# Optimization experiments

Measured on AMD Instinct MI355X. Metric: run time of the kernel, lower is better.

## Reference

```python
import jax, jax.numpy as jnp
import numpy as np

UNITS = 1024
IN_DIM = 1024
B, T = 32, 2048


def setup_inputs() -> dict:
    key = jax.random.key(0)
    k1, k2, k3 = jax.random.split(key, 3)
    # glorot-uniform style scaling for weights
    lim_k = float(np.sqrt(6.0 / (IN_DIM + UNITS)))
    lim_r = float(np.sqrt(6.0 / (UNITS + UNITS)))
    x = jax.random.normal(k1, (B, T, IN_DIM), dtype=jnp.float32)
    kernel = jax.random.uniform(k2, (IN_DIM, UNITS), minval=-lim_k, maxval=lim_k, dtype=jnp.float32)
    recurrent_kernel = jax.random.uniform(k3, (UNITS, UNITS), minval=-lim_r, maxval=lim_r, dtype=jnp.float32)
    h0 = jnp.zeros((B, UNITS), dtype=jnp.float32)
    return {"x": x, "h0": h0, "kernel": kernel, "recurrent_kernel": recurrent_kernel}


def reference(x, h0, kernel, recurrent_kernel):
    # MinimalRNNCell: h_t = x_t @ W_in + h_{t-1} @ W_rec (purely linear, no activation)
    # Hoist the input projection out of the scan: one big GEMM over [B*T, IN_DIM].
    xin = jnp.einsum('btd,du->btu', x, kernel)  # [B, T, U]

    def step(h, xt):
        h_new = xt + h @ recurrent_kernel
        return h_new, None

    # scan over time axis; Keras RNN default returns the last output [B, U]
    h_last, _ = jax.lax.scan(step, h0, jnp.swapaxes(xin, 0, 1))
    return h_last
```

## Files before the change

### kernel.cpp

```cpp
#include <hip/hip_runtime.h>
#include <cstddef>
#include <cstdint>


namespace {

constexpr int BATCH = 32;
constexpr int T = 2048;
constexpr int U = 1024;
constexpr int LJ = 8;
constexpr int CJ = T / LJ;
constexpr int MJ = CJ * BATCH;

typedef _Float16 f16;
typedef _Float16 f16x4 __attribute__((ext_vector_type(4)));
typedef _Float16 f16x8 __attribute__((ext_vector_type(8)));
typedef float f32x4 __attribute__((ext_vector_type(4)));

__device__ inline void gload16(const void* g, void* l) {
    __builtin_amdgcn_global_load_lds(
        (const __attribute__((address_space(1))) unsigned int*)g,
        (__attribute__((address_space(3))) unsigned int*)l, 16, 0, 0);
}

__global__ __launch_bounds__(256)
void split_x(const float* __restrict__ x, f16* __restrict__ xh, long n4)
{
    long i = (long)blockIdx.x * 256 + threadIdx.x;
    const long stride = (long)gridDim.x * 256;
    for (; i < n4; i += stride) {
        const float4 v = *(const float4*)(x + i * 4);
        f16x4 h;
        h.x = (f16)v.x; h.y = (f16)v.y; h.z = (f16)v.z; h.w = (f16)v.w;
        *(f16x4*)(xh + i * 4) = h;
    }
}

__global__ __launch_bounds__(256)
void prep(const float* __restrict__ R, const float* __restrict__ W,
          const float* __restrict__ h0,
          f16* __restrict__ TTRh, f16* __restrict__ TTRl,
          f16* __restrict__ Rrh, f16* __restrict__ Rrl,
          f16* __restrict__ GhT, f16* __restrict__ GlT,
          f16* __restrict__ Wrh, f16* __restrict__ Wrl,
          f16* __restrict__ h0rh, f16* __restrict__ h0rl)
{
    const int z = blockIdx.z;
    const float* S = z ? W : R;
    f16* Dh = z ? GhT : TTRh;
    f16* Dl = z ? GlT : TTRl;
    const long dstride = z ? 8192 : 1024;
    const long doff = z ? 7168 : 0;
    f16* Rh_ = z ? Wrh : Rrh;
    f16* Rl_ = z ? Wrl : Rrl;

    __shared__ float tile[32][33];
    const int t = threadIdx.x;
    const int k0 = blockIdx.x * 32;
    const int n0 = blockIdx.y * 32;
    {
        const int r = t >> 3, c4 = (t & 7) << 2;
        const float4 v = *(const float4*)(S + (size_t)(k0 + r) * U + n0 + c4);
        tile[r][c4 + 0] = v.x; tile[r][c4 + 1] = v.y;
        tile[r][c4 + 2] = v.z; tile[r][c4 + 3] = v.w;
        f16x4 h, lo;
        h.x = (f16)v.x; lo.x = (f16)((v.x - (float)h.x) * 2048.0f);
        h.y = (f16)v.y; lo.y = (f16)((v.y - (float)h.y) * 2048.0f);
        h.z = (f16)v.z; lo.z = (f16)((v.z - (float)h.z) * 2048.0f);
        h.w = (f16)v.w; lo.w = (f16)((v.w - (float)h.w) * 2048.0f);
        const size_t ro = (size_t)(k0 + r) * U + n0 + c4;
        *(f16x4*)(Rh_ + ro) = h;
        *(f16x4*)(Rl_ + ro) = lo;
    }
    __syncthreads();
    {
        const int c = t >> 3, r4 = (t & 7) << 2;
        float v0 = tile[r4 + 0][c], v1 = tile[r4 + 1][c],
              v2 = tile[r4 + 2][c], v3 = tile[r4 + 3][c];
        f16x4 h, lo;
        h.x = (f16)v0; lo.x = (f16)((v0 - (float)h.x) * 2048.0f);
        h.y = (f16)v1; lo.y = (f16)((v1 - (float)h.y) * 2048.0f);
        h.z = (f16)v2; lo.z = (f16)((v2 - (float)h.z) * 2048.0f);
        h.w = (f16)v3; lo.w = (f16)((v3 - (float)h.w) * 2048.0f);
        const size_t o = (size_t)(n0 + c) * dstride + doff + k0 + r4;
        *(f16x4*)(Dh + o) = h;
        *(f16x4*)(Dl + o) = lo;
    }
    if (z == 1 && blockIdx.x == 0) {
        const int r = t >> 3, c4 = (t & 7) << 2;
        const float4 v = *(const float4*)(h0 + (size_t)r * U + n0 + c4);
        f16x4 h, lo;
        h.x = (f16)v.x; lo.x = (f16)((v.x - (float)h.x) * 2048.0f);
        h.y = (f16)v.y; lo.y = (f16)((v.y - (float)h.y) * 2048.0f);
        h.z = (f16)v.z; lo.z = (f16)((v.z - (float)h.z) * 2048.0f);
        h.w = (f16)v.w; lo.w = (f16)((v.w - (float)h.w) * 2048.0f);
        const size_t ro = (size_t)r * U + n0 + c4;
        *(f16x4*)(h0rh + ro) = h;
        *(f16x4*)(h0rl + ro) = lo;
    }
}

__global__ __launch_bounds__(512, 2)
void main4(const f16* __restrict__ xh, const f16* __restrict__ GhT,
           const f16* __restrict__ GlT, float* __restrict__ g0,
           f16* __restrict__ g0rh, f16* __restrict__ g0rl)
{
    __shared__ __align__(16) f16 LA[2][16384];
    __shared__ __align__(16) f16 LBh[2][8192];
    __shared__ __align__(16) f16 LBl[2][8192];

    const int tid  = threadIdx.x;
    const int lane = tid & 63;
    const int w    = tid >> 6;
    const int wm   = w >> 1;
    const int wn   = w & 1;
    const int r0   = blockIdx.x * 256;
    const int c0   = blockIdx.y * 128;

    const int ch  = tid & 7;
    const int rid = tid >> 3;

    size_t aof[4];
    #pragma unroll
    for (int q = 0; q < 4; ++q) {
        const int m = q * 64 + rid;
        const int arow = r0 + m;
        const size_t xbase = ((size_t)(arow & 31) * T + (size_t)(arow >> 5) * LJ) * U;
        aof[q] = xbase * 2 + (size_t)((ch ^ (m & 7)) << 4);
    }
    size_t bof[2];
    #pragma unroll
    for (int q = 0; q < 2; ++q) {
        const int c = q * 64 + rid;
        bof[q] = ((size_t)(c0 + c) << 14) + (size_t)((ch ^ (c & 7)) << 4);
    }
    const int dst = tid << 4;

    f32x4 hh[4][4], xx[4][4];
    #pragma unroll
    for (int mi = 0; mi < 4; ++mi)
        #pragma unroll
        for (int ni = 0; ni < 4; ++ni) {
            hh[mi][ni] = (f32x4){0.f, 0.f, 0.f, 0.f};
            xx[mi][ni] = (f32x4){0.f, 0.f, 0.f, 0.f};
        }

    auto stage = [&](int b, int kt) {
        const size_t kb = (size_t)kt << 7;
        #pragma unroll
        for (int q = 0; q < 4; ++q)
            gload16((const char*)xh + aof[q] + kb, (char*)&LA[b][0] + q * 8192 + dst);
        #pragma unroll
        for (int q = 0; q < 2; ++q) {
            gload16((const char*)GhT + bof[q] + kb, (char*)&LBh[b][0] + q * 8192 + dst);
            gload16((const char*)GlT + bof[q] + kb, (char*)&LBl[b][0] + q * 8192 + dst);
        }
    };

    stage(0, 0);
    __syncthreads();

    int buf = 0;
    #pragma unroll 1
    for (int kt = 0; kt < 128; ++kt) {
        if (kt + 1 < 128) stage(buf ^ 1, kt + 1);

        #pragma unroll
        for (int ks = 0; ks < 2; ++ks) {
            const int kg = ks * 4 + (lane >> 4);
            f16x8 af[4], bh[4], bl[4];
            #pragma unroll
            for (int mi = 0; mi < 4; ++mi) {
                const int rr = wm * 64 + mi * 16 + (lane & 15);
                const int byte = rr * 128 + ((kg ^ (rr & 7)) << 4);
                af[mi] = *(const f16x8*)((const char*)&LA[buf][0] + byte);
            }
            #pragma unroll
            for (int ni = 0; ni < 4; ++ni) {
                const int cc = wn * 64 + ni * 16 + (lane & 15);
                const int byte = cc * 128 + ((kg ^ (cc & 7)) << 4);
                bh[ni] = *(const f16x8*)((const char*)&LBh[buf][0] + byte);
                bl[ni] = *(const f16x8*)((const char*)&LBl[buf][0] + byte);
            }
            #pragma unroll
            for (int mi = 0; mi < 4; ++mi)
                #pragma unroll
                for (int ni = 0; ni < 4; ++ni) {
                    hh[mi][ni] = __builtin_amdgcn_mfma_f32_16x16x32_f16(af[mi], bh[ni], hh[mi][ni], 0, 0, 0);
                    xx[mi][ni] = __builtin_amdgcn_mfma_f32_16x16x32_f16(af[mi], bl[ni], xx[mi][ni], 0, 0, 0);
                }
        }
        __syncthreads();
        buf ^= 1;
    }

    #pragma unroll
    for (int mi = 0; mi < 4; ++mi)
        #pragma unroll
        for (int ni = 0; ni < 4; ++ni) {
            const int col = c0 + wn * 64 + ni * 16 + (lane & 15);
            #pragma unroll
            for (int r = 0; r < 4; ++r) {
                const int row = r0 + wm * 64 + mi * 16 + ((lane >> 4) << 2) + r;
                const float val = hh[mi][ni][r] + xx[mi][ni][r] * (1.0f / 2048.0f);
                const size_t o = (size_t)row * U + col;
                g0[o] = val;
                const f16 hv = (f16)val;
                g0rh[o] = hv;
                g0rl[o] = (f16)((val - (float)hv) * 2048.0f);
            }
        }
}

struct MDesc {
    const f16* Ah; const f16* Al;
    const f16* BhT; const f16* BlT;
    const float* Aadd;
    float* C;
    f16* EhT; f16* ElT;
    f16* Rh; f16* Rl;
    long estride, eoff;
    int M;
    int amode;
    int cmode;
    float cscale, escale, fescale;
};

__global__ __launch_bounds__(256, 2)
void mk2(MDesc d0, MDesc d1)
{
    MDesc d = blockIdx.z ? d1 : d0;
    const int r0 = blockIdx.y * 128;
    if (r0 >= d.M) return;
    const int c0 = blockIdx.x * 64;

    __shared__ __align__(16) f16 SMEM[24576];
    f16 (*LAs)[2][4096] = (f16(*)[2][4096])(&SMEM[0]);
    f16 (*LBs)[2][2048] = (f16(*)[2][2048])(&SMEM[16384]);

    const int tid = threadIdx.x;
    const int lane = tid & 63;
    const int w = tid >> 6;
    const int wm = w >> 1, wn = w & 1;

    size_t asrc[2]; int adst[2];
    #pragma unroll
    for (int i = 0; i < 2; ++i) {
        const int c = tid + 256 * i;
        const int prow = c >> 3;
        const int chn = (c & 7) ^ (prow & 7);
        const int row = 2 * prow + (chn >> 2);
        int gr = r0 + row;
        if (gr >= d.M) gr = d.M - 1;
        const int ar = (d.amode == 2) ? (((gr >> 5) << 6) + (gr & 31)) : gr;
        asrc[i] = (size_t)ar * 2048 + (size_t)((chn & 3) << 4);
        adst[i] = c * 16;
    }
    const int bprow = tid >> 3;
    const int bchn = (tid & 7) ^ (bprow & 7);
    const size_t bsrc = (size_t)(c0 + 2 * bprow + (bchn >> 2)) * 2048
                      + (size_t)((bchn & 3) << 4);
    const int bdst = tid * 16;

    f32x4 hh[4][2], xx[4][2];
    #pragma unroll
    for (int mi = 0; mi < 4; ++mi)
        #pragma unroll
        for (int ni = 0; ni < 2; ++ni) {
            hh[mi][ni] = (f32x4){0.f, 0.f, 0.f, 0.f};
            xx[mi][ni] = (f32x4){0.f, 0.f, 0.f, 0.f};
        }

    auto stage = [&](int b, int kt) {
        const size_t kb = (size_t)kt << 6;
        #pragma unroll
        for (int i = 0; i < 2; ++i) {
            gload16((const char*)d.Ah + asrc[i] + kb, (char*)&LAs[b][0][0] + adst[i]);
            gload16((const char*)d.Al + asrc[i] + kb, (char*)&LAs[b][1][0] + adst[i]);
        }
        gload16((const char*)d.BhT + bsrc + kb, (char*)&LBs[b][0][0] + bdst);
        gload16((const char*)d.BlT + bsrc + kb, (char*)&LBs[b][1][0] + bdst);
    };

    stage(0, 0);
    __syncthreads();

    int buf = 0;
    #pragma unroll 1
    for (int kt = 0; kt < 32; ++kt) {
        if (kt + 1 < 32) stage(buf ^ 1, kt + 1);

        {
            const int kg = lane >> 4;
            f16x8 ah[4], al[4], bh[2], bl[2];
            #pragma unroll
            for (int mi = 0; mi < 4; ++mi) {
                const int rr = wm * 64 + mi * 16 + (lane & 15);
                const int prow = rr >> 1;
                const int chn = 4 * (rr & 1) + kg;
                const int byte = prow * 128 + ((chn ^ (prow & 7)) << 4);
                ah[mi] = *(const f16x8*)((const char*)&LAs[buf][0][0] + byte);
                al[mi] = *(const f16x8*)((const char*)&LAs[buf][1][0] + byte);
            }
            #pragma unroll
            for (int ni = 0; ni < 2; ++ni) {
                const int cc = wn * 32 + ni * 16 + (lane & 15);
                const int prow = cc >> 1;
                const int chn = 4 * (cc & 1) + kg;
                const int byte = prow * 128 + ((chn ^ (prow & 7)) << 4);
                bh[ni] = *(const f16x8*)((const char*)&LBs[buf][0][0] + byte);
                bl[ni] = *(const f16x8*)((const char*)&LBs[buf][1][0] + byte);
            }
            #pragma unroll
            for (int mi = 0; mi < 4; ++mi)
                #pragma unroll
                for (int ni = 0; ni < 2; ++ni) {
                    hh[mi][ni] = __builtin_amdgcn_mfma_f32_16x16x32_f16(ah[mi], bh[ni], hh[mi][ni], 0, 0, 0);
                    xx[mi][ni] = __builtin_amdgcn_mfma_f32_16x16x32_f16(ah[mi], bl[ni], xx[mi][ni], 0, 0, 0);
                    xx[mi][ni] = __builtin_amdgcn_mfma_f32_16x16x32_f16(al[mi], bh[ni], xx[mi][ni], 0, 0, 0);
                }
        }
        __syncthreads();
        buf ^= 1;
    }

    const bool temit = (d.EhT != nullptr);
    f16* Ehs = &SMEM[0];
    f16* Els = &SMEM[8192];

    #pragma unroll
    for (int mi = 0; mi < 4; ++mi) {
        #pragma unroll
        for (int ni = 0; ni < 2; ++ni) {
            const int orow = wm * 64 + mi * 16 + ((lane >> 4) << 2);
            const int colL = wn * 32 + ni * 16 + (lane & 15);
            const int col  = c0 + colL;
            float o[4];
            #pragma unroll
            for (int r = 0; r < 4; ++r) {
                o[r] = (hh[mi][ni][r] + xx[mi][ni][r] * (1.0f / 2048.0f)) * d.cscale;
                const int grow = r0 + orow + r;
                if (grow < d.M) {
                    if (d.amode == 2) {
                        const int arow2 = (((grow >> 5) << 6) + (grow & 31)) + 32;
                        o[r] += d.Aadd[(size_t)arow2 * U + col];
                    }
                    if (d.C) {
                        float* cp = d.C + (size_t)grow * U + col;
                        if (d.cmode == 1) o[r] += *cp;
                        *cp = o[r];
                    }
                    if (d.Rh) {
                        const float e = o[r] * d.fescale;
                        const f16 hv = (f16)e;
                        d.Rh[(size_t)grow * U + col] = hv;
                        d.Rl[(size_t)grow * U + col] = (f16)((e - (float)hv) * 2048.0f);
                    }
                }
            }
            if (temit && (r0 + orow) < d.M) {
                f16x4 h4, l4;
                #pragma unroll
                for (int r = 0; r < 4; ++r) {
                    const float e = o[r] * d.escale;
                    h4[r] = (f16)e;
                    l4[r] = (f16)((e - (float)h4[r]) * 2048.0f);
                }
                const int blk = orow >> 3;
                const int boff = colL * 256 + ((blk ^ (colL & 15)) << 4) + (orow & 7) * 2;
                *(f16x4*)((char*)Ehs + boff) = h4;
                *(f16x4*)((char*)Els + boff) = l4;
            }
        }
    }

    if (temit) {
        __syncthreads();
        const int c  = tid & 63;
        const int b0 = (tid >> 6) * 4;
        const size_t gbase = (size_t)(c0 + c) * d.estride + d.eoff + (size_t)r0;
        #pragma unroll
        for (int i = 0; i < 4; ++i) {
            const int blk = b0 + i;
            const int off = c * 256 + ((blk ^ (c & 15)) << 4);
            *(f16x8*)(d.EhT + gbase + blk * 8) = *(const f16x8*)((char*)Ehs + off);
            *(f16x8*)(d.ElT + gbase + blk * 8) = *(const f16x8*)((char*)Els + off);
        }
    }
}

}

extern "C" void kernel_launch(void* const* d_in, const int* in_sizes, int n_in,
                              void* d_out, int out_size, void* d_ws, size_t ws_size,
                              hipStream_t stream) {
    const float* x  = (const float*)d_in[0];
    const float* h0 = (const float*)d_in[1];
    const float* W  = (const float*)d_in[2];
    const float* R  = (const float*)d_in[3];
    float* out = (float*)d_out;

    const size_t M1 = (size_t)1024 * 1024;
    float* g0 = (float*)d_ws;
    float* gA = g0 + 8 * M1;
    float* gB = gA + 4 * M1;
    f16* fp = (f16*)(gB + 4 * M1);
    auto take = [&](size_t n) { f16* r = fp; fp += n; return r; };
    f16* xh   = take(64 * M1);
    f16* GhT  = take(8 * M1);
    f16* GlT  = take(8 * M1);
    f16* Tqh[8]; f16* Tql[8];
    for (int l = 0; l < 8; ++l) { Tqh[l] = take(M1); Tql[l] = take(M1); }
    f16* Qrh[7]; f16* Qrl[7];
    for (int l = 0; l < 7; ++l) { Qrh[l] = take(M1); Qrl[l] = take(M1); }
    f16* Gfrh = take(4 * M1); f16* Gfrl = take(4 * M1);
    f16* h0rh = take(32 * 1024); f16* h0rl = take(32 * 1024);
    f16* g0rh = take(8 * M1); f16* g0rl = take(8 * M1);
    f16* gArh = take(4 * M1); f16* gArl = take(4 * M1);
    f16* gBrh = take(4 * M1); f16* gBrl = take(4 * M1);
    f16* TTRh = Tqh[3]; f16* TTRl = Tql[3];
    f16* TT1h = Tqh[1]; f16* TT1l = Tql[1];
    f16* TT2h = Tqh[2]; f16* TT2l = Tql[2];
    f16* Rrh  = Qrh[3]; f16* Rrl  = Qrl[3];
    f16* R2rh = Qrh[1]; f16* R2rl = Qrl[1];
    f16* R4rh = Qrh[2]; f16* R4rl = Qrl[2];

    auto MD2 = [](const f16* Ah, const f16* Al, const f16* Bh, const f16* Bl,
                  const float* Aadd, float* C, f16* Eh, f16* El, long eoff, long estride,
                  f16* Rh, f16* Rl, int M, int amode, int cmode,
                  float cs, float es, float fs) {
        MDesc d;
        d.Ah = Ah; d.Al = Al; d.BhT = Bh; d.BlT = Bl; d.Aadd = Aadd; d.C = C;
        d.EhT = Eh; d.ElT = El; d.Rh = Rh; d.Rl = Rl;
        d.estride = estride; d.eoff = eoff; d.M = M; d.amode = amode; d.cmode = cmode;
        d.cscale = cs; d.escale = es; d.fescale = fs;
        return d;
    };
    MDesc dz = MD2(nullptr, nullptr, nullptr, nullptr, nullptr, nullptr,
                   nullptr, nullptr, 0, 1024, nullptr, nullptr, 0, 0, 0, 1.f, 1.f, 1.f);
    auto PAIR = [&](MDesc a, MDesc b) {
        int y0 = (a.M + 127) >> 7, y1 = (b.M + 127) >> 7;
        int y = y0 > y1 ? y0 : y1; if (y < 1) y = 1;
        mk2<<<dim3(16, (unsigned)y, 2), 256, 0, stream>>>(a, b);
    };

    split_x<<<2048, 256, 0, stream>>>(x, xh, (long)BATCH * T * U / 4);
    prep<<<dim3(32, 32, 2), 256, 0, stream>>>(R, W, h0, TTRh, TTRl, Rrh, Rrl,
                                              GhT, GlT,
                                              Gfrh + 3 * M1, Gfrl + 3 * M1,
                                              h0rh, h0rl);

    PAIR(MD2(Rrh, Rrl, TTRh, TTRl, nullptr, nullptr, TT1h, TT1l, 0, 1024,
             R2rh, R2rl, U, 0, 0, 1.f, 1.f, 1.f),
         MD2(Gfrh + 3 * M1, Gfrl + 3 * M1, TTRh, TTRl, nullptr, nullptr,
             GhT, GlT, 6144, 8192, Gfrh + 2 * M1, Gfrl + 2 * M1, U, 0, 0, 1.f, 1.f, 1.f));
    PAIR(MD2(R2rh, R2rl, TT1h, TT1l, nullptr, nullptr, TT2h, TT2l, 0, 1024,
             R4rh, R4rl, U, 0, 0, 1.f, 1.f, 1.f),
         MD2(Gfrh + 2 * M1, Gfrl + 2 * M1, TT1h, TT1l, nullptr, nullptr,
             GhT, GlT, 4096, 8192, Gfrh, Gfrl, 2 * U, 0, 0, 1.f, 1.f, 1.f));
    PAIR(MD2(R4rh, R4rl, TT2h, TT2l, nullptr, nullptr, Tqh[0], Tql[0], 0, 1024,
             Qrh[0], Qrl[0], U, 0, 0, 1.f, 1.f, 1.f),
         MD2(Gfrh, Gfrl, TT2h, TT2l, nullptr, nullptr,
             GhT, GlT, 0, 8192, nullptr, nullptr, 4 * U, 0, 0, 1.f, 1.f, 1.f));

    main4<<<dim3(32, 8), 512, 0, stream>>>(xh, GhT, GlT, g0, g0rh, g0rl);

    PAIR(MD2(h0rh, h0rl, Tqh[0], Tql[0], nullptr, g0, nullptr, nullptr, 0, 1024,
             g0rh, g0rl, BATCH, 0, 1, 1.f, 1.f, 1.f),
         MD2(Qrh[0], Qrl[0], Tqh[0], Tql[0], nullptr, nullptr, Tqh[1], Tql[1], 0, 1024,
             Qrh[1], Qrl[1], U, 0, 0, 1.f, 1.f, 1.f));

    const float aS[9] = {1.f, 1.f, 1.f, 1.f, 1.f,
                         0.015625f, 9.5367431640625e-07f, 7.105427357601002e-15f, 0.f};
    const float cS[8] = {1.f, 1.f, 1.f, 1.f, 1.f,
                         64.f, 68719476736.f, 1.5474250491067253e26f};
    float* gcur = g0; f16* gcrh = g0rh; f16* gcrl = g0rl;
    float* gnxt = gA; f16* gnrh = gArh; f16* gnrl = gArl;
    float* gprv = gB; f16* gprh = gBrh; f16* gprl = gBrl;
    for (int l = 0; l < 8; ++l) {
        const int M = BATCH * ((CJ / 2) >> l);
        MDesc dc = MD2(gcrh, gcrl, Tqh[l], Tql[l], gcur, (l == 7) ? out : gnxt,
                       nullptr, nullptr, 0, 1024,
                       (l < 7) ? gnrh : nullptr, (l < 7) ? gnrl : nullptr,
                       M, 2, 0, cS[l], 1.f, aS[l + 1]);
        MDesc dq = dz;
        if (l < 6) {
            const int s = l + 1;
            const float fe = (s == 5) ? 5.960464477539063e-08f : 1.f;
            const float te = (s == 5) ? 1.52587890625e-05f : 1.f;
            f16* reh = (s + 1 <= 6) ? Qrh[s + 1] : nullptr;
            f16* rel = (s + 1 <= 6) ? Qrl[s + 1] : nullptr;
            dq = MD2(Qrh[s], Qrl[s], Tqh[s], Tql[s], nullptr, nullptr,
                     Tqh[s + 1], Tql[s + 1], 0, 1024, reh, rel, U, 0, 0, 1.f, te, fe);
        }
        PAIR(dc, dq);
        float* tf = gprv; gprv = gcur; gcur = gnxt; gnxt = tf;
        f16* th = gprh; f16* tl = gprl;
        gprh = gcrh; gprl = gcrl;
        gcrh = gnrh; gcrl = gnrl;
        gnrh = th;   gnrl = tl;
    }
    (void)in_sizes; (void)n_in; (void)out_size; (void)ws_size;
}
```

Baseline: 802.4 us.

## Overlap x fp16 conversion with power GEMMs and deepen load pipeline to three stages

The standalone split_x kernel is removed. Its fp32-to-fp16 conversion of x is split into three chunks, each handled by an extra z-slice of blocks in the first three mk2 launches, so the conversion runs alongside the small matrix-power GEMMs instead of serially before them. Separately, main4 and mk2 now keep two tiles of global-to-LDS loads in flight, using explicit vmcnt waits and raw barriers in place of the single-ahead double buffer with __syncthreads. The risks are that the conversion blocks compete with the GEMM blocks for bandwidth and CUs, and that the hand-written vmcnt counts must exactly match the number of loads issued per stage.

```diff
diff --git a/kernel.cpp b/kernel.cpp
--- a/kernel.cpp
+++ b/kernel.cpp
@@ -21,19 +21,6 @@
     __builtin_amdgcn_global_load_lds(
         (const __attribute__((address_space(1))) unsigned int*)g,
         (__attribute__((address_space(3))) unsigned int*)l, 16, 0, 0);
-}
-
-__global__ __launch_bounds__(256)
-void split_x(const float* __restrict__ x, f16* __restrict__ xh, long n4)
-{
-    long i = (long)blockIdx.x * 256 + threadIdx.x;
-    const long stride = (long)gridDim.x * 256;
-    for (; i < n4; i += stride) {
-        const float4 v = *(const float4*)(x + i * 4);
-        f16x4 h;
-        h.x = (f16)v.x; h.y = (f16)v.y; h.z = (f16)v.z; h.w = (f16)v.w;
-        *(f16x4*)(xh + i * 4) = h;
-    }
 }
 
 __global__ __launch_bounds__(256)
@@ -158,13 +145,16 @@
     };
 
     stage(0, 0);
-    __syncthreads();
-
-    int buf = 0;
+    stage(1, 1);
+
     #pragma unroll 1
     for (int kt = 0; kt < 128; ++kt) {
-        if (kt + 1 < 128) stage(buf ^ 1, kt + 1);
-
+        if (kt < 127) asm volatile("s_waitcnt vmcnt(8)" ::: "memory");
+        else          asm volatile("s_waitcnt vmcnt(0)" ::: "memory");
+        __builtin_amdgcn_s_barrier();
+        asm volatile("" ::: "memory");
+
+        const int buf = kt & 1;
         #pragma unroll
         for (int ks = 0; ks < 2; ++ks) {
             const int kg = ks * 4 + (lane >> 4);
@@ -190,8 +180,11 @@
                     xx[mi][ni] = __builtin_amdgcn_mfma_f32_16x16x32_f16(af[mi], bl[ni], xx[mi][ni], 0, 0, 0);
                 }
         }
-        __syncthreads();
-        buf ^= 1;
+
+        asm volatile("" ::: "memory");
+        __builtin_amdgcn_s_barrier();
+        asm volatile("" ::: "memory");
+        if (kt + 2 < 128) stage(buf, kt + 2);
     }
 
     #pragma unroll
@@ -227,8 +220,22 @@
 };
 
 __global__ __launch_bounds__(256, 2)
-void mk2(MDesc d0, MDesc d1)
+void mk2(MDesc d0, MDesc d1,
+         const float* __restrict__ xsrc, f16* __restrict__ xdst, long q0, long q1)
 {
+    if (blockIdx.z == 2) {
+        const long nb = (long)gridDim.x * gridDim.y;
+        long i = q0 + ((long)blockIdx.y * gridDim.x + blockIdx.x) * 256 + threadIdx.x;
+        const long stride = nb * 256;
+        for (; i < q1; i += stride) {
+            const float4 v = *(const float4*)(xsrc + i * 4);
+            f16x4 h;
+            h.x = (f16)v.x; h.y = (f16)v.y; h.z = (f16)v.z; h.w = (f16)v.w;
+            *(f16x4*)(xdst + i * 4) = h;
+        }
+        return;
+    }
+
     MDesc d = blockIdx.z ? d1 : d0;
     const int r0 = blockIdx.y * 128;
     if (r0 >= d.M) return;
@@ -283,13 +290,16 @@
     };
 
     stage(0, 0);
-    __syncthreads();
-
-    int buf = 0;
+    stage(1, 1);
+
     #pragma unroll 1
     for (int kt = 0; kt < 32; ++kt) {
-        if (kt + 1 < 32) stage(buf ^ 1, kt + 1);
-
+        if (kt < 31) asm volatile("s_waitcnt vmcnt(6)" ::: "memory");
+        else         asm volatile("s_waitcnt vmcnt(0)" ::: "memory");
+        __builtin_amdgcn_s_barrier();
+        asm volatile("" ::: "memory");
+
+        const int buf = kt & 1;
         {
             const int kg = lane >> 4;
             f16x8 ah[4], al[4], bh[2], bl[2];
@@ -320,8 +330,11 @@
                     xx[mi][ni] = __builtin_amdgcn_mfma_f32_16x16x32_f16(al[mi], bh[ni], xx[mi][ni], 0, 0, 0);
                 }
         }
-        __syncthreads();
-        buf ^= 1;
+
+        asm volatile("" ::: "memory");
+        __builtin_amdgcn_s_barrier();
+        asm volatile("" ::: "memory");
+        if (kt + 2 < 32) stage(buf, kt + 2);
     }
 
     const bool temit = (d.EhT != nullptr);
@@ -438,37 +451,43 @@
     };
     MDesc dz = MD2(nullptr, nullptr, nullptr, nullptr, nullptr, nullptr,
                    nullptr, nullptr, 0, 1024, nullptr, nullptr, 0, 0, 0, 1.f, 1.f, 1.f);
-    auto PAIR = [&](MDesc a, MDesc b) {
+    auto PAIR = [&](MDesc a, MDesc b, long q0, long q1) {
         int y0 = (a.M + 127) >> 7, y1 = (b.M + 127) >> 7;
         int y = y0 > y1 ? y0 : y1; if (y < 1) y = 1;
-        mk2<<<dim3(16, (unsigned)y, 2), 256, 0, stream>>>(a, b);
+        const unsigned z = (q1 > q0) ? 3u : 2u;
+        mk2<<<dim3(16, (unsigned)y, z), 256, 0, stream>>>(a, b, x, xh, q0, q1);
     };
 
-    split_x<<<2048, 256, 0, stream>>>(x, xh, (long)BATCH * T * U / 4);
     prep<<<dim3(32, 32, 2), 256, 0, stream>>>(R, W, h0, TTRh, TTRl, Rrh, Rrl,
                                               GhT, GlT,
                                               Gfrh + 3 * M1, Gfrl + 3 * M1,
                                               h0rh, h0rl);
 
+    const long n4 = (long)BATCH * T * U / 4;
+    const long t1 = n4 / 3, t2 = 2 * n4 / 3;
     PAIR(MD2(Rrh, Rrl, TTRh, TTRl, nullptr, nullptr, TT1h, TT1l, 0, 1024,
              R2rh, R2rl, U, 0, 0, 1.f, 1.f, 1.f),
          MD2(Gfrh + 3 * M1, Gfrl + 3 * M1, TTRh, TTRl, nullptr, nullptr,
-             GhT, GlT, 6144, 8192, Gfrh + 2 * M1, Gfrl + 2 * M1, U, 0, 0, 1.f, 1.f, 1.f));
+             GhT, GlT, 6144, 8192, Gfrh + 2 * M1, Gfrl + 2 * M1, U, 0, 0, 1.f, 1.f, 1.f),
+         0, t1);
     PAIR(MD2(R2rh, R2rl, TT1h, TT1l, nullptr, nullptr, TT2h, TT2l, 0, 1024,
              R4rh, R4rl, U, 0, 0, 1.f, 1.f, 1.f),
          MD2(Gfrh + 2 * M1, Gfrl + 2 * M1, TT1h, TT1l, nullptr, nullptr,
-             GhT, GlT, 4096, 8192, Gfrh, Gfrl, 2 * U, 0, 0, 1.f, 1.f, 1.f));
+             GhT, GlT, 4096, 8192, Gfrh, Gfrl, 2 * U, 0, 0, 1.f, 1.f, 1.f),
+         t1, t2);
     PAIR(MD2(R4rh, R4rl, TT2h, TT2l, nullptr, nullptr, Tqh[0], Tql[0], 0, 1024,
              Qrh[0], Qrl[0], U, 0, 0, 1.f, 1.f, 1.f),
          MD2(Gfrh, Gfrl, TT2h, TT2l, nullptr, nullptr,
-             GhT, GlT, 0, 8192, nullptr, nullptr, 4 * U, 0, 0, 1.f, 1.f, 1.f));
+             GhT, GlT, 0, 8192, nullptr, nullptr, 4 * U, 0, 0, 1.f, 1.f, 1.f),
+         t2, n4);
 
     main4<<<dim3(32, 8), 512, 0, stream>>>(xh, GhT, GlT, g0, g0rh, g0rl);
 
     PAIR(MD2(h0rh, h0rl, Tqh[0], Tql[0], nullptr, g0, nullptr, nullptr, 0, 1024,
              g0rh, g0rl, BATCH, 0, 1, 1.f, 1.f, 1.f),
          MD2(Qrh[0], Qrl[0], Tqh[0], Tql[0], nullptr, nullptr, Tqh[1], Tql[1], 0, 1024,
-             Qrh[1], Qrl[1], U, 0, 0, 1.f, 1.f, 1.f));
+             Qrh[1], Qrl[1], U, 0, 0, 1.f, 1.f, 1.f),
+         0, 0);
 
     const float aS[9] = {1.f, 1.f, 1.f, 1.f, 1.f,
                          0.015625f, 9.5367431640625e-07f, 7.105427357601002e-15f, 0.f};
@@ -493,7 +512,7 @@
             dq = MD2(Qrh[s], Qrl[s], Tqh[s], Tql[s], nullptr, nullptr,
                      Tqh[s + 1], Tql[s + 1], 0, 1024, reh, rel, U, 0, 0, 1.f, te, fe);
         }
-        PAIR(dc, dq);
+        PAIR(dc, dq, 0, 0);
         float* tf = gprv; gprv = gcur; gcur = gnxt; gnxt = tf;
         f16* th = gprh; f16* tl = gprl;
         gprh = gcrh; gprl = gcrl;
```

Result: slower. 835.9 us (+4.2%).

## Merge chained GEMM launches into persistent cooperative kernels; deepen main4 prefetch

Applied to the files above, without the earlier changes.

The many small paired GEMM launches (setup chain and the log-depth tail) are replaced by two persistent cooperative kernels that walk a list of stages with grid-wide syncs in between. This removes per-launch overhead and the tail effect of each launch. It falls back to per-stage launches if the cooperative launch fails. Separately, main4's K loop now prefetches two stages ahead using explicit vmcnt waits and raw barriers instead of __syncthreads. The risks are grid.sync cost, and a 512-block cooperative grid that needs two blocks resident per CU.

```diff
diff --git a/kernel.cpp b/kernel.cpp
--- a/kernel.cpp
+++ b/kernel.cpp
@@ -1,4 +1,5 @@
 #include <hip/hip_runtime.h>
+#include <hip/hip_cooperative_groups.h>
 #include <cstddef>
 #include <cstdint>
 
@@ -16,6 +17,8 @@
 typedef _Float16 f16x4 __attribute__((ext_vector_type(4)));
 typedef _Float16 f16x8 __attribute__((ext_vector_type(8)));
 typedef float f32x4 __attribute__((ext_vector_type(4)));
+
+namespace cg = cooperative_groups;
 
 __device__ inline void gload16(const void* g, void* l) {
     __builtin_amdgcn_global_load_lds(
@@ -158,13 +161,16 @@
     };
 
     stage(0, 0);
-    __syncthreads();
-
-    int buf = 0;
+    stage(1, 1);
+
     #pragma unroll 1
     for (int kt = 0; kt < 128; ++kt) {
-        if (kt + 1 < 128) stage(buf ^ 1, kt + 1);
-
+        if (kt < 127) asm volatile("s_waitcnt vmcnt(8)" ::: "memory");
+        else          asm volatile("s_waitcnt vmcnt(0)" ::: "memory");
+        __builtin_amdgcn_s_barrier();
+        asm volatile("" ::: "memory");
+
+        const int buf = kt & 1;
         #pragma unroll
         for (int ks = 0; ks < 2; ++ks) {
             const int kg = ks * 4 + (lane >> 4);
@@ -190,8 +196,11 @@
                     xx[mi][ni] = __builtin_amdgcn_mfma_f32_16x16x32_f16(af[mi], bl[ni], xx[mi][ni], 0, 0, 0);
                 }
         }
-        __syncthreads();
-        buf ^= 1;
+
+        asm volatile("" ::: "memory");
+        __builtin_amdgcn_s_barrier();
+        asm volatile("" ::: "memory");
+        if (kt + 2 < 128) stage(buf, kt + 2);
     }
 
     #pragma unroll
@@ -226,15 +235,16 @@
     float cscale, escale, fescale;
 };
 
-__global__ __launch_bounds__(256, 2)
-void mk2(MDesc d0, MDesc d1)
+struct TaskStage { MDesc j0, j1; int ny0, ny1; };
+struct KArgs { TaskStage st[9]; int nst; };
+
+__device__ void gemm_body(const MDesc& d, int xc, int yr, f16* SMEM)
 {
-    MDesc d = blockIdx.z ? d1 : d0;
-    const int r0 = blockIdx.y * 128;
+    __syncthreads();
+    const int r0 = yr * 128;
     if (r0 >= d.M) return;
-    const int c0 = blockIdx.x * 64;
-
-    __shared__ __align__(16) f16 SMEM[24576];
+    const int c0 = xc * 64;
+
     f16 (*LAs)[2][4096] = (f16(*)[2][4096])(&SMEM[0]);
     f16 (*LBs)[2][2048] = (f16(*)[2][2048])(&SMEM[16384]);
 
@@ -271,7 +281,7 @@
             xx[mi][ni] = (f32x4){0.f, 0.f, 0.f, 0.f};
         }
 
-    auto stage = [&](int b, int kt) {
+    auto stg = [&](int b, int kt) {
         const size_t kb = (size_t)kt << 6;
         #pragma unroll
         for (int i = 0; i < 2; ++i) {
@@ -282,13 +292,13 @@
         gload16((const char*)d.BlT + bsrc + kb, (char*)&LBs[b][1][0] + bdst);
     };
 
-    stage(0, 0);
+    stg(0, 0);
     __syncthreads();
 
     int buf = 0;
     #pragma unroll 1
     for (int kt = 0; kt < 32; ++kt) {
-        if (kt + 1 < 32) stage(buf ^ 1, kt + 1);
+        if (kt + 1 < 32) stg(buf ^ 1, kt + 1);
 
         {
             const int kg = lane >> 4;
@@ -386,6 +396,39 @@
             *(f16x8*)(d.EhT + gbase + blk * 8) = *(const f16x8*)((char*)Ehs + off);
             *(f16x8*)(d.ElT + gbase + blk * 8) = *(const f16x8*)((char*)Els + off);
         }
+    }
+}
+
+__global__ __launch_bounds__(256, 2)
+void stagesk(KArgs a)
+{
+    __shared__ __align__(16) f16 SMEM[24576];
+    cg::grid_group grid = cg::this_grid();
+    for (int s = 0; s < a.nst; ++s) {
+        const TaskStage& st = a.st[s];
+        const int n0 = 16 * st.ny0;
+        const int ntasks = n0 + 16 * st.ny1;
+        for (int t = blockIdx.x; t < ntasks; t += gridDim.x) {
+            const bool first = (t < n0);
+            const MDesc& d = first ? st.j0 : st.j1;
+            const int tt = first ? t : t - n0;
+            gemm_body(d, tt & 15, tt >> 4, SMEM);
+        }
+        grid.sync();
+    }
+}
+
+__global__ __launch_bounds__(256, 2)
+void stage1k(TaskStage st)
+{
+    __shared__ __align__(16) f16 SMEM[24576];
+    const int n0 = 16 * st.ny0;
+    const int ntasks = n0 + 16 * st.ny1;
+    for (int t = blockIdx.x; t < ntasks; t += gridDim.x) {
+        const bool first = (t < n0);
+        const MDesc& d = first ? st.j0 : st.j1;
+        const int tt = first ? t : t - n0;
+        gemm_body(d, tt & 15, tt >> 4, SMEM);
     }
 }
 
@@ -438,67 +481,100 @@
     };
     MDesc dz = MD2(nullptr, nullptr, nullptr, nullptr, nullptr, nullptr,
                    nullptr, nullptr, 0, 1024, nullptr, nullptr, 0, 0, 0, 1.f, 1.f, 1.f);
-    auto PAIR = [&](MDesc a, MDesc b) {
-        int y0 = (a.M + 127) >> 7, y1 = (b.M + 127) >> 7;
-        int y = y0 > y1 ? y0 : y1; if (y < 1) y = 1;
-        mk2<<<dim3(16, (unsigned)y, 2), 256, 0, stream>>>(a, b);
+    auto ST = [](MDesc a, int ya, MDesc b, int yb) {
+        TaskStage s; s.j0 = a; s.ny0 = ya; s.j1 = b; s.ny1 = yb; return s;
     };
 
-    split_x<<<2048, 256, 0, stream>>>(x, xh, (long)BATCH * T * U / 4);
+    KArgs chainA; chainA.nst = 3;
+    chainA.st[0] = ST(
+        MD2(Rrh, Rrl, TTRh, TTRl, nullptr, nullptr, TT1h, TT1l, 0, 1024,
+            R2rh, R2rl, U, 0, 0, 1.f, 1.f, 1.f), 8,
+        MD2(Gfrh + 3 * M1, Gfrl + 3 * M1, TTRh, TTRl, nullptr, nullptr,
+            GhT, GlT, 6144, 8192, Gfrh + 2 * M1, Gfrl + 2 * M1, U, 0, 0, 1.f, 1.f, 1.f), 8);
+    chainA.st[1] = ST(
+        MD2(R2rh, R2rl, TT1h, TT1l, nullptr, nullptr, TT2h, TT2l, 0, 1024,
+            R4rh, R4rl, U, 0, 0, 1.f, 1.f, 1.f), 8,
+        MD2(Gfrh + 2 * M1, Gfrl + 2 * M1, TT1h, TT1l, nullptr, nullptr,
+            GhT, GlT, 4096, 8192, Gfrh, Gfrl, 2 * U, 0, 0, 1.f, 1.f, 1.f), 16);
+    chainA.st[2] = ST(
+        MD2(R4rh, R4rl, TT2h, TT2l, nullptr, nullptr, Tqh[0], Tql[0], 0, 1024,
+            Qrh[0], Qrl[0], U, 0, 0, 1.f, 1.f, 1.f), 8,
+        MD2(Gfrh, Gfrl, TT2h, TT2l, nullptr, nullptr,
+            GhT, GlT, 0, 8192, nullptr, nullptr, 4 * U, 0, 0, 1.f, 1.f, 1.f), 32);
+
+    KArgs tailA; tailA.nst = 9;
+    tailA.st[0] = ST(
+        MD2(h0rh, h0rl, Tqh[0], Tql[0], nullptr, g0, nullptr, nullptr, 0, 1024,
+            g0rh, g0rl, BATCH, 0, 1, 1.f, 1.f, 1.f), 1,
+        MD2(Qrh[0], Qrl[0], Tqh[0], Tql[0], nullptr, nullptr, Tqh[1], Tql[1], 0, 1024,
+            Qrh[1], Qrl[1], U, 0, 0, 1.f, 1.f, 1.f), 8);
+
+    const float aS[9] = {1.f, 1.f, 1.f, 1.f, 1.f,
+                         0.015625f, 9.5367431640625e-07f, 7.105427357601002e-15f, 0.f};
+    const float cS[8] = {1.f, 1.f, 1.f, 1.f, 1.f,
+                         64.f, 68719476736.f, 1.5474250491067253e26f};
+    {
+        float* gcur = g0; f16* gcrh = g0rh; f16* gcrl = g0rl;
+        float* gnxt = gA; f16* gnrh = gArh; f16* gnrl = gArl;
+        float* gprv = gB; f16* gprh = gBrh; f16* gprl = gBrl;
+        for (int l = 0; l < 8; ++l) {
+            const int M = BATCH * ((CJ / 2) >> l);
+            MDesc dc = MD2(gcrh, gcrl, Tqh[l], Tql[l], gcur, (l == 7) ? out : gnxt,
+                           nullptr, nullptr, 0, 1024,
+                           (l < 7) ? gnrh : nullptr, (l < 7) ? gnrl : nullptr,
+                           M, 2, 0, cS[l], 1.f, aS[l + 1]);
+            MDesc dq = dz;
+            int yq = 0;
+            if (l < 6) {
+                const int s = l + 1;
+                const float fe = (s == 5) ? 5.960464477539063e-08f : 1.f;
+                const float te = (s == 5) ? 1.52587890625e-05f : 1.f;
+                f16* reh = (s + 1 <= 6) ? Qrh[s + 1] : nullptr;
+                f16* rel = (s + 1 <= 6) ? Qrl[s + 1] : nullptr;
+                dq = MD2(Qrh[s], Qrl[s], Tqh[s], Tql[s], nullptr, nullptr,
+                         Tqh[s + 1], Tql[s + 1], 0, 1024, reh, rel, U, 0, 0, 1.f, te, fe);
+                yq = 8;
+            }
+            tailA.st[1 + l] = ST(dc, (M + 127) >> 7, dq, yq);
+            float* tf = gprv; gprv = gcur; gcur = gnxt; gnxt = tf;
+            f16* th = gprh; f16* tl = gprl;
+            gprh = gcrh; gprl = gcrl;
+            gcrh = gnrh; gcrl = gnrl;
+            gnrh = th;   gnrl = tl;
+        }
+    }
+
     prep<<<dim3(32, 32, 2), 256, 0, stream>>>(R, W, h0, TTRh, TTRl, Rrh, Rrl,
                                               GhT, GlT,
                                               Gfrh + 3 * M1, Gfrl + 3 * M1,
                                               h0rh, h0rl);
-
-    PAIR(MD2(Rrh, Rrl, TTRh, TTRl, nullptr, nullptr, TT1h, TT1l, 0, 1024,
-             R2rh, R2rl, U, 0, 0, 1.f, 1.f, 1.f),
-         MD2(Gfrh + 3 * M1, Gfrl + 3 * M1, TTRh, TTRl, nullptr, nullptr,
-             GhT, GlT, 6144, 8192, Gfrh + 2 * M1, Gfrl + 2 * M1, U, 0, 0, 1.f, 1.f, 1.f));
-    PAIR(MD2(R2rh, R2rl, TT1h, TT1l, nullptr, nullptr, TT2h, TT2l, 0, 1024,
-             R4rh, R4rl, U, 0, 0, 1.f, 1.f, 1.f),
-         MD2(Gfrh + 2 * M1, Gfrl + 2 * M1, TT1h, TT1l, nullptr, nullptr,
-             GhT, GlT, 4096, 8192, Gfrh, Gfrl, 2 * U, 0, 0, 1.f, 1.f, 1.f));
-    PAIR(MD2(R4rh, R4rl, TT2h, TT2l, nullptr, nullptr, Tqh[0], Tql[0], 0, 1024,
-             Qrh[0], Qrl[0], U, 0, 0, 1.f, 1.f, 1.f),
-         MD2(Gfrh, Gfrl, TT2h, TT2l, nullptr, nullptr,
-             GhT, GlT, 0, 8192, nullptr, nullptr, 4 * U, 0, 0, 1.f, 1.f, 1.f));
+    split_x<<<2048, 256, 0, stream>>>(x, xh, (long)BATCH * T * U / 4);
+
+    bool coop_ok = true;
+    {
+        void* ka[] = { (void*)&chainA };
+        hipError_t rc = hipLaunchCooperativeKernel((const void*)&stagesk,
+                                                   dim3(512), dim3(256), ka, 0, stream);
+        if (rc != hipSuccess) coop_ok = false;
+    }
+    if (!coop_ok) {
+        for (int s = 0; s < chainA.nst; ++s)
+            stage1k<<<dim3(512), 256, 0, stream>>>(chainA.st[s]);
+    }
 
     main4<<<dim3(32, 8), 512, 0, stream>>>(xh, GhT, GlT, g0, g0rh, g0rl);
 
-    PAIR(MD2(h0rh, h0rl, Tqh[0], Tql[0], nullptr, g0, nullptr, nullptr, 0, 1024,
-             g0rh, g0rl, BATCH, 0, 1, 1.f, 1.f, 1.f),
-         MD2(Qrh[0], Qrl[0], Tqh[0], Tql[0], nullptr, nullptr, Tqh[1], Tql[1], 0, 1024,
-             Qrh[1], Qrl[1], U, 0, 0, 1.f, 1.f, 1.f));
-
-    const float aS[9] = {1.f, 1.f, 1.f, 1.f, 1.f,
-                         0.015625f, 9.5367431640625e-07f, 7.105427357601002e-15f, 0.f};
-    const float cS[8] = {1.f, 1.f, 1.f, 1.f, 1.f,
-                         64.f, 68719476736.f, 1.5474250491067253e26f};
-    float* gcur = g0; f16* gcrh = g0rh; f16* gcrl = g0rl;
-    float* gnxt = gA; f16* gnrh = gArh; f16* gnrl = gArl;
-    float* gprv = gB; f16* gprh = gBrh; f16* gprl = gBrl;
-    for (int l = 0; l < 8; ++l) {
-        const int M = BATCH * ((CJ / 2) >> l);
-        MDesc dc = MD2(gcrh, gcrl, Tqh[l], Tql[l], gcur, (l == 7) ? out : gnxt,
-                       nullptr, nullptr, 0, 1024,
-                       (l < 7) ? gnrh : nullptr, (l < 7) ? gnrl : nullptr,
-                       M, 2, 0, cS[l], 1.f, aS[l + 1]);
-        MDesc dq = dz;
-        if (l < 6) {
-            const int s = l + 1;
-            const float fe = (s == 5) ? 5.960464477539063e-08f : 1.f;
-            const float te = (s == 5) ? 1.52587890625e-05f : 1.f;
-            f16* reh = (s + 1 <= 6) ? Qrh[s + 1] : nullptr;
-            f16* rel = (s + 1 <= 6) ? Qrl[s + 1] : nullptr;
-            dq = MD2(Qrh[s], Qrl[s], Tqh[s], Tql[s], nullptr, nullptr,
-                     Tqh[s + 1], Tql[s + 1], 0, 1024, reh, rel, U, 0, 0, 1.f, te, fe);
-        }
-        PAIR(dc, dq);
-        float* tf = gprv; gprv = gcur; gcur = gnxt; gnxt = tf;
-        f16* th = gprh; f16* tl = gprl;
-        gprh = gcrh; gprl = gcrl;
-        gcrh = gnrh; gcrl = gnrl;
-        gnrh = th;   gnrl = tl;
+    if (coop_ok) {
+        void* ka[] = { (void*)&tailA };
+        hipError_t rc = hipLaunchCooperativeKernel((const void*)&stagesk,
+                                                   dim3(512), dim3(256), ka, 0, stream);
+        if (rc != hipSuccess) coop_ok = false;
+        if (!coop_ok)
+            for (int s = 0; s < tailA.nst; ++s)
+                stage1k<<<dim3(512), 256, 0, stream>>>(tailA.st[s]);
+    } else {
+        for (int s = 0; s < tailA.nst; ++s)
+            stage1k<<<dim3(512), 256, 0, stream>>>(tailA.st[s]);
     }
     (void)in_sizes; (void)n_in; (void)out_size; (void)ws_size;
 }
```

Result: slower. 1.554 ms (+93.6%).

## Deepen LDS prefetch to two stages and double K-tile in mk2

Applied to the files above, without the earlier changes.

Both GEMM kernels switch from load-then-sync double buffering to a two-tile-ahead prefetch. Each iteration waits with explicit vmcnt counts and raw s_barrier instead of a full __syncthreads, so global-to-LDS loads for tile kt+2 overlap the MFMA work on tile kt. mk2 also doubles its K tile from 64 to 128, doubling LDS use, and drops launch bounds to one block per SM, trading occupancy for fewer loop iterations and barriers. The split_x launch is reordered after prep.

```diff
diff --git a/kernel.cpp b/kernel.cpp
--- a/kernel.cpp
+++ b/kernel.cpp
@@ -158,13 +158,16 @@
     };
 
     stage(0, 0);
-    __syncthreads();
-
-    int buf = 0;
+    stage(1, 1);
+
     #pragma unroll 1
     for (int kt = 0; kt < 128; ++kt) {
-        if (kt + 1 < 128) stage(buf ^ 1, kt + 1);
-
+        if (kt < 127) asm volatile("s_waitcnt vmcnt(8)" ::: "memory");
+        else          asm volatile("s_waitcnt vmcnt(0)" ::: "memory");
+        __builtin_amdgcn_s_barrier();
+        asm volatile("" ::: "memory");
+
+        const int buf = kt & 1;
         #pragma unroll
         for (int ks = 0; ks < 2; ++ks) {
             const int kg = ks * 4 + (lane >> 4);
@@ -190,8 +193,11 @@
                     xx[mi][ni] = __builtin_amdgcn_mfma_f32_16x16x32_f16(af[mi], bl[ni], xx[mi][ni], 0, 0, 0);
                 }
         }
-        __syncthreads();
-        buf ^= 1;
+
+        asm volatile("" ::: "memory");
+        __builtin_amdgcn_s_barrier();
+        asm volatile("" ::: "memory");
+        if (kt + 2 < 128) stage(buf, kt + 2);
     }
 
     #pragma unroll
@@ -226,7 +232,7 @@
     float cscale, escale, fescale;
 };
 
-__global__ __launch_bounds__(256, 2)
+__global__ __launch_bounds__(256, 1)
 void mk2(MDesc d0, MDesc d1)
 {
     MDesc d = blockIdx.z ? d1 : d0;
@@ -234,33 +240,36 @@
     if (r0 >= d.M) return;
     const int c0 = blockIdx.x * 64;
 
-    __shared__ __align__(16) f16 SMEM[24576];
-    f16 (*LAs)[2][4096] = (f16(*)[2][4096])(&SMEM[0]);
-    f16 (*LBs)[2][2048] = (f16(*)[2][2048])(&SMEM[16384]);
+    __shared__ __align__(16) f16 SMEM[49152];
+    f16 (*LAs)[2][8192] = (f16(*)[2][8192])(&SMEM[0]);
+    f16 (*LBs)[2][4096] = (f16(*)[2][4096])(&SMEM[32768]);
 
     const int tid = threadIdx.x;
     const int lane = tid & 63;
     const int w = tid >> 6;
     const int wm = w >> 1, wn = w & 1;
 
-    size_t asrc[2]; int adst[2];
+    size_t asrc[4]; int adst[4];
+    #pragma unroll
+    for (int i = 0; i < 4; ++i) {
+        const int c = tid + 256 * i;
+        const int prow = c >> 3;
+        const int chn = (c & 7) ^ (prow & 7);
+        int gr = r0 + prow;
+        if (gr >= d.M) gr = d.M - 1;
+        const int ar = (d.amode == 2) ? (((gr >> 5) << 6) + (gr & 31)) : gr;
+        asrc[i] = (size_t)ar * 2048 + (size_t)(chn << 4);
+        adst[i] = c * 16;
+    }
+    size_t bsrc[2]; int bdst[2];
     #pragma unroll
     for (int i = 0; i < 2; ++i) {
         const int c = tid + 256 * i;
         const int prow = c >> 3;
         const int chn = (c & 7) ^ (prow & 7);
-        const int row = 2 * prow + (chn >> 2);
-        int gr = r0 + row;
-        if (gr >= d.M) gr = d.M - 1;
-        const int ar = (d.amode == 2) ? (((gr >> 5) << 6) + (gr & 31)) : gr;
-        asrc[i] = (size_t)ar * 2048 + (size_t)((chn & 3) << 4);
-        adst[i] = c * 16;
-    }
-    const int bprow = tid >> 3;
-    const int bchn = (tid & 7) ^ (bprow & 7);
-    const size_t bsrc = (size_t)(c0 + 2 * bprow + (bchn >> 2)) * 2048
-                      + (size_t)((bchn & 3) << 4);
-    const int bdst = tid * 16;
+        bsrc[i] = (size_t)(c0 + prow) * 2048 + (size_t)(chn << 4);
+        bdst[i] = c * 16;
+    }
 
     f32x4 hh[4][2], xx[4][2];
     #pragma unroll
@@ -271,43 +280,46 @@
             xx[mi][ni] = (f32x4){0.f, 0.f, 0.f, 0.f};
         }
 
-    auto stage = [&](int b, int kt) {
-        const size_t kb = (size_t)kt << 6;
-        #pragma unroll
-        for (int i = 0; i < 2; ++i) {
+    auto stg = [&](int b, int kt) {
+        const size_t kb = (size_t)kt << 7;
+        #pragma unroll
+        for (int i = 0; i < 4; ++i) {
             gload16((const char*)d.Ah + asrc[i] + kb, (char*)&LAs[b][0][0] + adst[i]);
             gload16((const char*)d.Al + asrc[i] + kb, (char*)&LAs[b][1][0] + adst[i]);
         }
-        gload16((const char*)d.BhT + bsrc + kb, (char*)&LBs[b][0][0] + bdst);
-        gload16((const char*)d.BlT + bsrc + kb, (char*)&LBs[b][1][0] + bdst);
+        #pragma unroll
+        for (int i = 0; i < 2; ++i) {
+            gload16((const char*)d.BhT + bsrc[i] + kb, (char*)&LBs[b][0][0] + bdst[i]);
+            gload16((const char*)d.BlT + bsrc[i] + kb, (char*)&LBs[b][1][0] + bdst[i]);
+        }
     };
 
-    stage(0, 0);
-    __syncthreads();
-
-    int buf = 0;
+    stg(0, 0);
+    stg(1, 1);
+
     #pragma unroll 1
-    for (int kt = 0; kt < 32; ++kt) {
-        if (kt + 1 < 32) stage(buf ^ 1, kt + 1);
-
-        {
-            const int kg = lane >> 4;
+    for (int kt = 0; kt < 16; ++kt) {
+        if (kt < 15) asm volatile("s_waitcnt vmcnt(12)" ::: "memory");
+        else         asm volatile("s_waitcnt vmcnt(0)" ::: "memory");
+        __builtin_amdgcn_s_barrier();
+        asm volatile("" ::: "memory");
+
+        const int buf = kt & 1;
+        #pragma unroll
+        for (int ks = 0; ks < 2; ++ks) {
+            const int kg = ks * 4 + (lane >> 4);
             f16x8 ah[4], al[4], bh[2], bl[2];
             #pragma unroll
             for (int mi = 0; mi < 4; ++mi) {
                 const int rr = wm * 64 + mi * 16 + (lane & 15);
-                const int prow = rr >> 1;
-                const int chn = 4 * (rr & 1) + kg;
-                const int byte = prow * 128 + ((chn ^ (prow & 7)) << 4);
+                const int byte = rr * 128 + ((kg ^ (rr & 7)) << 4);
                 ah[mi] = *(const f16x8*)((const char*)&LAs[buf][0][0] + byte);
                 al[mi] = *(const f16x8*)((const char*)&LAs[buf][1][0] + byte);
             }
             #pragma unroll
             for (int ni = 0; ni < 2; ++ni) {
                 const int cc = wn * 32 + ni * 16 + (lane & 15);
-                const int prow = cc >> 1;
-                const int chn = 4 * (cc & 1) + kg;
-                const int byte = prow * 128 + ((chn ^ (prow & 7)) << 4);
+                const int byte = cc * 128 + ((kg ^ (cc & 7)) << 4);
                 bh[ni] = *(const f16x8*)((const char*)&LBs[buf][0][0] + byte);
                 bl[ni] = *(const f16x8*)((const char*)&LBs[buf][1][0] + byte);
             }
@@ -320,8 +332,11 @@
                     xx[mi][ni] = __builtin_amdgcn_mfma_f32_16x16x32_f16(al[mi], bh[ni], xx[mi][ni], 0, 0, 0);
                 }
         }
-        __syncthreads();
-        buf ^= 1;
+
+        asm volatile("" ::: "memory");
+        __builtin_amdgcn_s_barrier();
+        asm volatile("" ::: "memory");
+        if (kt + 2 < 16) stg(buf, kt + 2);
     }
 
     const bool temit = (d.EhT != nullptr);
@@ -444,11 +459,11 @@
         mk2<<<dim3(16, (unsigned)y, 2), 256, 0, stream>>>(a, b);
     };
 
-    split_x<<<2048, 256, 0, stream>>>(x, xh, (long)BATCH * T * U / 4);
     prep<<<dim3(32, 32, 2), 256, 0, stream>>>(R, W, h0, TTRh, TTRl, Rrh, Rrl,
                                               GhT, GlT,
                                               Gfrh + 3 * M1, Gfrl + 3 * M1,
                                               h0rh, h0rl);
+    split_x<<<2048, 256, 0, stream>>>(x, xh, (long)BATCH * T * U / 4);
 
     PAIR(MD2(Rrh, Rrl, TTRh, TTRl, nullptr, nullptr, TT1h, TT1l, 0, 1024,
              R2rh, R2rl, U, 0, 0, 1.f, 1.f, 1.f),
```

Measured after the change: 803.1 us. About the same (+0.1%).
